# Optimization experiments

Measured on AMD Instinct MI355X. Metric: run time of the kernel, lower is better.

Reference implementation:

```python
import jax, jax.numpy as jnp
import numpy as np

N = 20000
E = 640000
H, C = 4, 64
L = 3
B = 16
EPS = 1e-5


def setup_inputs() -> dict:
    key = jax.random.key(0)
    ks = jax.random.split(key, 12)
    x = jax.random.normal(ks[0], (N, 256), dtype=jnp.float32)
    edge_index = jax.random.randint(ks[1], (2, E), 0, N, dtype=jnp.int64)
    batch = jnp.sort(jax.random.randint(ks[2], (N,), 0, B, dtype=jnp.int64))
    s = 0.05
    return {
        "x": x,
        "edge_index": edge_index,
        "batch": batch,
        "Wl": jax.random.normal(ks[3], (L, 256, H * C), dtype=jnp.float32) * s,
        "bl": jnp.zeros((L, H * C), dtype=jnp.float32),
        "Wr": jax.random.normal(ks[4], (L, 256, H * C), dtype=jnp.float32) * s,
        "br": jnp.zeros((L, H * C), dtype=jnp.float32),
        "att": jax.random.normal(ks[5], (L, H, C), dtype=jnp.float32) * s,
        "conv_bias": jnp.zeros((L, H * C), dtype=jnp.float32),
        "prelu_a": jnp.full((L,), 0.25, dtype=jnp.float32),
        "norm_w": jnp.ones((H * C,), dtype=jnp.float32),
        "norm_b": jnp.zeros((H * C,), dtype=jnp.float32),
        "norm_alpha": jnp.ones((H * C,), dtype=jnp.float32),
        "fc_W": jax.random.normal(ks[6], (H * C, 128), dtype=jnp.float32) * s,
        "fc_b": jnp.zeros((128,), dtype=jnp.float32),
    }


def graph_norm(h, w, b, alpha):
    # GraphNorm with batch=None: all rows form one segment (as in source forward)
    mean = jnp.mean(h, axis=0, keepdims=True)
    shifted = h - alpha * mean
    var = jnp.mean(shifted * shifted, axis=0, keepdims=True)
    return w * shifted / jnp.sqrt(var + EPS) + b


def gatv2_layer(h, src, dst, Wl, bl, Wr, br, att, bias):
    xl = (h @ Wl + bl).reshape(N, H, C)  # source transform
    xr = (h @ Wr + br).reshape(N, H, C)  # target transform
    m = jax.nn.leaky_relu(xl[src] + xr[dst], negative_slope=0.2)  # [Etot,H,C]
    e = jnp.einsum("ehc,hc->eh", m, att)  # [Etot,H]
    emax = jax.ops.segment_max(e, dst, num_segments=N)  # self-loops guarantee coverage
    ex = jnp.exp(e - emax[dst])
    denom = jax.ops.segment_sum(ex, dst, num_segments=N)
    alpha = ex / denom[dst]
    out = jax.ops.segment_sum(alpha[:, :, None] * xl[src], dst, num_segments=N)
    return out.reshape(N, H * C) + bias


def reference(x, edge_index, batch, Wl, bl, Wr, br, att, conv_bias, prelu_a,
              norm_w, norm_b, norm_alpha, fc_W, fc_b):
    loop = jnp.arange(N, dtype=edge_index.dtype)
    src = jnp.concatenate([edge_index[0], loop])  # add self-loops (PyG default)
    dst = jnp.concatenate([edge_index[1], loop])
    h = x
    for l in range(L):
        h = gatv2_layer(h, src, dst, Wl[l], bl[l], Wr[l], br[l], att[l], conv_bias[l])
        h = graph_norm(h, norm_w, norm_b, norm_alpha)
        h = jnp.where(h >= 0, h, prelu_a[l] * h)  # PReLU; dropout is identity in eval
    pooled = jax.ops.segment_sum(h, batch, num_segments=B)  # global_add_pool
    pooled = graph_norm(pooled, norm_w, norm_b, norm_alpha)  # shared norm reused after pool
    return pooled @ fc_W + fc_b
```

## Files before the change

### kernel.cpp

```cpp
#include <hip/hip_runtime.h>
#include <math.h>

#define N_NODES 20000
#define N_EDGES 640000
#define ETOT (N_EDGES + N_NODES)
#define HC 256
#define NLAYER 3
#define NBATCH 16
#define GEPS 1e-5f
#define STAT_BLOCKS 256

typedef unsigned short u16;
typedef unsigned int u32;
typedef __attribute__((ext_vector_type(8))) short short8;
typedef __attribute__((ext_vector_type(4))) float floatx4;

__device__ __forceinline__ u16 f2bf(float f) {
    u32 u = __float_as_uint(f);
    u32 r = (u + 0x7FFFu + ((u >> 16) & 1u)) >> 16;
    return (u16)r;
}

__device__ __forceinline__ float4 bf2f4(uint2 u) {
    float4 r;
    r.x = __uint_as_float(u.x << 16);
    r.y = __uint_as_float(u.x & 0xFFFF0000u);
    r.z = __uint_as_float(u.y << 16);
    r.w = __uint_as_float(u.y & 0xFFFF0000u);
    return r;
}

__device__ __forceinline__ float dpp_red16(float x) {
    x += __int_as_float(__builtin_amdgcn_update_dpp(0, __float_as_int(x), 0xB1, 0xF, 0xF, true));
    x += __int_as_float(__builtin_amdgcn_update_dpp(0, __float_as_int(x), 0x4E, 0xF, 0xF, true));
    x += __int_as_float(__builtin_amdgcn_update_dpp(0, __float_as_int(x), 0x141, 0xF, 0xF, true));
    x += __int_as_float(__builtin_amdgcn_update_dpp(0, __float_as_int(x), 0x140, 0xF, 0xF, true));
    return x;
}


__global__ void init_deg(int* deg) {
    int i = blockIdx.x * 256 + threadIdx.x;
    if (i < N_NODES) deg[i] = 1;
}

__global__ void count_deg(const int* __restrict__ dst, int* __restrict__ deg) {
    int e = blockIdx.x * 256 + threadIdx.x;
    if (e < N_EDGES) atomicAdd(&deg[dst[e]], 1);
}

__global__ __launch_bounds__(1024) void scan_excl(int* __restrict__ data, int* __restrict__ cursor) {
    __shared__ int wsum[16];
    __shared__ int carry_s;
    int tid = threadIdx.x, lane = tid & 63, wid = tid >> 6;
    if (tid == 0) carry_s = 0;
    __syncthreads();
    for (int base = 0; base < N_NODES; base += 1024) {
        int i = base + tid;
        int v = (i < N_NODES) ? data[i] : 0;
        int x = v;
        #pragma unroll
        for (int off = 1; off < 64; off <<= 1) {
            int t = __shfl_up(x, off);
            if (lane >= off) x += t;
        }
        if (lane == 63) wsum[wid] = x;
        __syncthreads();
        int carry = carry_s;
        __syncthreads();
        if (tid == 0) {
            int run = 0;
            #pragma unroll
            for (int w2 = 0; w2 < 16; ++w2) { int t = wsum[w2]; wsum[w2] = run; run += t; }
            carry_s = carry + run;
        }
        __syncthreads();
        int excl = carry + wsum[wid] + x - v;
        if (i < N_NODES) { data[i] = excl; cursor[i] = excl; }
        __syncthreads();
    }
    if (tid == 0) data[N_NODES] = carry_s;
}

__global__ void scatter_edges(const int* __restrict__ src, const int* __restrict__ dst,
                              int* __restrict__ cursor, int* __restrict__ col) {
    int t = blockIdx.x * 256 + threadIdx.x;
    if (t < N_NODES) {
        int p = atomicAdd(&cursor[t], 1);
        col[p] = t;
    } else if (t < N_NODES + N_EDGES) {
        int e = t - N_NODES;
        int p = atomicAdd(&cursor[dst[e]], 1);
        col[p] = src[e];
    }
}


__global__ __launch_bounds__(256) void convert_x(const float* __restrict__ x, u16* __restrict__ xb) {
    int i = blockIdx.x * 256 + threadIdx.x;
    const float4* x4 = (const float4*)x + (size_t)i * 2;
    float4 a = x4[0], b = x4[1];
    u16 o[8] = {f2bf(a.x), f2bf(a.y), f2bf(a.z), f2bf(a.w),
                f2bf(b.x), f2bf(b.y), f2bf(b.z), f2bf(b.w)};
    *((uint4*)xb + i) = *(const uint4*)o;
}

__global__ void transpose_w(const float* __restrict__ Wl, const float* __restrict__ Wr,
                            u16* __restrict__ WT) {
    __shared__ float T[32][33];
    int l = blockIdx.z;
    int n0 = blockIdx.y * 32, k0 = blockIdx.x * 32;
    const float* W = ((n0 < 256) ? Wl : Wr) + (size_t)l * 65536;
    int nn = n0 & 255;
    int tx = threadIdx.x, ty = threadIdx.y;
    #pragma unroll
    for (int i = 0; i < 4; ++i)
        T[ty + i * 8][tx] = W[(size_t)(k0 + ty + i * 8) * 256 + nn + tx];
    __syncthreads();
    u16* out = WT + (size_t)l * 512 * 256;
    #pragma unroll
    for (int i = 0; i < 4; ++i)
        out[(size_t)(n0 + ty + i * 8) * 256 + k0 + tx] = f2bf(T[tx][ty + i * 8]);
}


__global__ __launch_bounds__(256) void gemm_mfma(
    const u16* __restrict__ Abf, const u16* __restrict__ WT,
    const float* __restrict__ b0, const float* __restrict__ b1,
    u16* __restrict__ xlb, float* __restrict__ xrf) {
    __shared__ u16 As[128][40];
    __shared__ u16 Bs[128][40];
    int row0 = blockIdx.x * 128;
    int nstrip = blockIdx.y;
    int ncol0 = nstrip * 128;
    const float* bias = (nstrip < 2) ? b0 : b1;

    int tid = threadIdx.x;
    int wave = tid >> 6, lane = tid & 63;
    int wm = (wave & 1) * 64, wn = (wave >> 1) * 64;
    int quad = lane >> 4, l16 = lane & 15;

    floatx4 acc[4][4] = {};

    int sr = tid >> 1;
    int sh = (tid & 1) * 16;

    for (int k0 = 0; k0 < 256; k0 += 32) {
        int gr = row0 + sr;
        uint4 av0 = make_uint4(0, 0, 0, 0), av1 = make_uint4(0, 0, 0, 0);
        if (gr < N_NODES) {
            const u16* p = Abf + (size_t)gr * 256 + k0 + sh;
            av0 = *(const uint4*)p;
            av1 = *(const uint4*)(p + 8);
        }
        const u16* q = WT + (size_t)(ncol0 + sr) * 256 + k0 + sh;
        uint4 bv0 = *(const uint4*)q;
        uint4 bv1 = *(const uint4*)(q + 8);
        *(uint4*)&As[sr][sh] = av0;
        *(uint4*)&As[sr][sh + 8] = av1;
        *(uint4*)&Bs[sr][sh] = bv0;
        *(uint4*)&Bs[sr][sh + 8] = bv1;
        __syncthreads();

        short8 af[4], bfr[4];
        #pragma unroll
        for (int mi = 0; mi < 4; ++mi)
            af[mi] = *(const short8*)&As[wm + mi * 16 + l16][quad * 8];
        #pragma unroll
        for (int ni = 0; ni < 4; ++ni)
            bfr[ni] = *(const short8*)&Bs[wn + ni * 16 + l16][quad * 8];
        #pragma unroll
        for (int mi = 0; mi < 4; ++mi)
            #pragma unroll
            for (int ni = 0; ni < 4; ++ni)
                acc[mi][ni] = __builtin_amdgcn_mfma_f32_16x16x32_bf16(af[mi], bfr[ni], acc[mi][ni], 0, 0, 0);
        __syncthreads();
    }

    if (nstrip < 2) {
        int c0 = nstrip * 128;
        #pragma unroll
        for (int ni = 0; ni < 4; ++ni) {
            int col = c0 + wn + ni * 16 + l16;
            float bv = bias[col];
            #pragma unroll
            for (int mi = 0; mi < 4; ++mi) {
                int gr = row0 + wm + mi * 16 + quad * 4;
                #pragma unroll
                for (int r = 0; r < 4; ++r) {
                    if (gr + r < N_NODES)
                        xlb[(size_t)(gr + r) * 256 + col] = f2bf(acc[mi][ni][r] + bv);
                }
            }
        }
    } else {
        int c0 = (nstrip - 2) * 128;
        #pragma unroll
        for (int ni = 0; ni < 4; ++ni) {
            int col = c0 + wn + ni * 16 + l16;
            float bv = bias[col];
            #pragma unroll
            for (int mi = 0; mi < 4; ++mi) {
                int gr = row0 + wm + mi * 16 + quad * 4;
                #pragma unroll
                for (int r = 0; r < 4; ++r) {
                    if (gr + r < N_NODES)
                        xrf[(size_t)(gr + r) * 256 + col] = acc[mi][ni][r] + bv;
                }
            }
        }
    }
}


__global__ __launch_bounds__(256) void gat_agg(
    const u16* __restrict__ xlb, const float* __restrict__ xr,
    const int* __restrict__ rowptr, const int* __restrict__ col,
    const float* __restrict__ att_l, const float* __restrict__ bias_l,
    float* __restrict__ out) {
    int wid = threadIdx.x >> 6, lane = threadIdx.x & 63;
    int node = blockIdx.x * 4 + wid;
    if (node >= N_NODES) return;
    const uint2* xl2 = (const uint2*)xlb;
    float4 attv = ((const float4*)att_l)[lane];
    float4 xrv = ((const float4*)xr)[(size_t)node * 64 + lane];
    int beg = rowptr[node], end = rowptr[node + 1];

    float denom = 0.f;
    float4 acc = make_float4(0.f, 0.f, 0.f, 0.f);

    int j = beg;
    for (; j + 8 <= end; j += 8) {
        int s[8];
        uint2 raw[8];
        float4 a[8];
        float p[8];
        #pragma unroll
        for (int u = 0; u < 8; ++u) s[u] = col[j + u];
        #pragma unroll
        for (int u = 0; u < 8; ++u) raw[u] = xl2[(size_t)s[u] * 64 + lane];
        #pragma unroll
        for (int u = 0; u < 8; ++u) {
            a[u] = bf2f4(raw[u]);
            float vx = a[u].x + xrv.x, vy = a[u].y + xrv.y;
            float vz = a[u].z + xrv.z, vw = a[u].w + xrv.w;
            vx = fmaxf(vx, 0.2f * vx);
            vy = fmaxf(vy, 0.2f * vy);
            vz = fmaxf(vz, 0.2f * vz);
            vw = fmaxf(vw, 0.2f * vw);
            p[u] = vx * attv.x + vy * attv.y + vz * attv.z + vw * attv.w;
        }
        #pragma unroll
        for (int u = 0; u < 8; ++u) p[u] = dpp_red16(p[u]);
        #pragma unroll
        for (int u = 0; u < 8; ++u) {
            float w = __expf(p[u]);
            denom += w;
            acc.x += w * a[u].x; acc.y += w * a[u].y;
            acc.z += w * a[u].z; acc.w += w * a[u].w;
        }
    }
    for (; j < end; ++j) {
        int s = col[j];
        float4 a = bf2f4(xl2[(size_t)s * 64 + lane]);
        float vx = a.x + xrv.x, vy = a.y + xrv.y;
        float vz = a.z + xrv.z, vw = a.w + xrv.w;
        vx = fmaxf(vx, 0.2f * vx);
        vy = fmaxf(vy, 0.2f * vy);
        vz = fmaxf(vz, 0.2f * vz);
        vw = fmaxf(vw, 0.2f * vw);
        float p = vx * attv.x + vy * attv.y + vz * attv.z + vw * attv.w;
        p = dpp_red16(p);
        float w = __expf(p);
        denom += w;
        acc.x += w * a.x; acc.y += w * a.y; acc.z += w * a.z; acc.w += w * a.w;
    }

    float inv = 1.f / denom;
    float4 b4 = ((const float4*)bias_l)[lane];
    float4 o;
    o.x = acc.x * inv + b4.x; o.y = acc.y * inv + b4.y;
    o.z = acc.z * inv + b4.z; o.w = acc.w * inv + b4.w;
    ((float4*)out)[(size_t)node * 64 + lane] = o;
}


__global__ __launch_bounds__(256) void col_stats_part(const float* __restrict__ h,
                                                      float* __restrict__ partials) {
    __shared__ float s_red[256][8];
    int t = threadIdx.x;
    int rgrp = t >> 6;
    int c4 = t & 63;
    float4 sum = make_float4(0.f, 0.f, 0.f, 0.f);
    float4 sq = make_float4(0.f, 0.f, 0.f, 0.f);
    for (int r = blockIdx.x * 4 + rgrp; r < N_NODES; r += STAT_BLOCKS * 4) {
        float4 v = ((const float4*)h)[(size_t)r * 64 + c4];
        sum.x += v.x; sum.y += v.y; sum.z += v.z; sum.w += v.w;
        sq.x += v.x * v.x; sq.y += v.y * v.y; sq.z += v.z * v.z; sq.w += v.w * v.w;
    }
    s_red[t][0] = sum.x; s_red[t][1] = sum.y; s_red[t][2] = sum.z; s_red[t][3] = sum.w;
    s_red[t][4] = sq.x;  s_red[t][5] = sq.y;  s_red[t][6] = sq.z;  s_red[t][7] = sq.w;
    __syncthreads();
    if (rgrp == 0) {
        float acc8[8];
        #pragma unroll
        for (int k = 0; k < 8; ++k)
            acc8[k] = s_red[c4][k] + s_red[64 + c4][k] + s_red[128 + c4][k] + s_red[192 + c4][k];
        float* pb = partials + (size_t)blockIdx.x * 512;
        *(float4*)&pb[c4 * 4]       = make_float4(acc8[0], acc8[1], acc8[2], acc8[3]);
        *(float4*)&pb[256 + c4 * 4] = make_float4(acc8[4], acc8[5], acc8[6], acc8[7]);
    }
}

__global__ __launch_bounds__(256) void stats_reduce(const float* __restrict__ partials,
                                                    float* __restrict__ stats) {
    int o = blockIdx.x * 256 + threadIdx.x;
    float s = 0.f;
    for (int b = 0; b < STAT_BLOCKS; ++b) s += partials[(size_t)b * 512 + o];
    stats[o] = s;
}


__global__ __launch_bounds__(256) void norm_prelu(
    const float* __restrict__ h2, u16* __restrict__ hbf, float* __restrict__ hf,
    const float* __restrict__ stats,
    const float* __restrict__ w, const float* __restrict__ b, const float* __restrict__ alpha,
    const float* __restrict__ pa, int l, int wf32) {
    int t = threadIdx.x;
    int row = blockIdx.x * 4 + (t >> 6);
    int c4 = t & 63;
    int c = c4 * 4;
    const float invn = 1.f / (float)N_NODES;
    float4 m4 = *(const float4*)&stats[c];
    float4 e4 = *(const float4*)&stats[256 + c];
    float4 al4 = *(const float4*)&alpha[c];
    float4 w4 = *(const float4*)&w[c];
    float4 b4 = *(const float4*)&b[c];
    float ap = pa[l];

    float4 mean, wc, sh;
    mean.x = m4.x * invn; mean.y = m4.y * invn; mean.z = m4.z * invn; mean.w = m4.w * invn;
    float4 Eh2;
    Eh2.x = e4.x * invn; Eh2.y = e4.y * invn; Eh2.z = e4.z * invn; Eh2.w = e4.w * invn;
    wc.x = w4.x * rsqrtf(Eh2.x - (2.f * al4.x - al4.x * al4.x) * mean.x * mean.x + GEPS);
    wc.y = w4.y * rsqrtf(Eh2.y - (2.f * al4.y - al4.y * al4.y) * mean.y * mean.y + GEPS);
    wc.z = w4.z * rsqrtf(Eh2.z - (2.f * al4.z - al4.z * al4.z) * mean.z * mean.z + GEPS);
    wc.w = w4.w * rsqrtf(Eh2.w - (2.f * al4.w - al4.w * al4.w) * mean.w * mean.w + GEPS);
    sh.x = al4.x * mean.x; sh.y = al4.y * mean.y; sh.z = al4.z * mean.z; sh.w = al4.w * mean.w;

    float4 v = ((const float4*)h2)[(size_t)row * 64 + c4];
    v.x = (v.x - sh.x) * wc.x + b4.x;
    v.y = (v.y - sh.y) * wc.y + b4.y;
    v.z = (v.z - sh.z) * wc.z + b4.z;
    v.w = (v.w - sh.w) * wc.w + b4.w;
    v.x = (v.x >= 0.f) ? v.x : ap * v.x;
    v.y = (v.y >= 0.f) ? v.y : ap * v.y;
    v.z = (v.z >= 0.f) ? v.z : ap * v.z;
    v.w = (v.w >= 0.f) ? v.w : ap * v.w;
    u16 o4[4] = {f2bf(v.x), f2bf(v.y), f2bf(v.z), f2bf(v.w)};
    *(uint2*)(hbf + (size_t)row * 256 + c) = *(const uint2*)o4;
    if (wf32) ((float4*)hf)[(size_t)row * 64 + c4] = v;
}


__global__ __launch_bounds__(256) void pool_kernel(const float* __restrict__ h,
                                                   const int* __restrict__ batch,
                                                   float* __restrict__ pooled) {
    __shared__ float accs[NBATCH][256];
    int c = threadIdx.x;
    #pragma unroll
    for (int b = 0; b < NBATCH; ++b) accs[b][c] = 0.f;
    int rows_per = (N_NODES + gridDim.x - 1) / gridDim.x;
    int r0 = blockIdx.x * rows_per;
    int r1 = min(N_NODES, r0 + rows_per);
    for (int i = r0; i < r1; ++i) accs[batch[i]][c] += h[(size_t)i * 256 + c];
    #pragma unroll
    for (int b = 0; b < NBATCH; ++b) atomicAdd(&pooled[b * 256 + c], accs[b][c]);
}

__global__ __launch_bounds__(256) void pool_norm(const float* __restrict__ pooled, float* __restrict__ pn,
                                                 const float* __restrict__ w, const float* __restrict__ b,
                                                 const float* __restrict__ alpha) {
    int c = threadIdx.x;
    float mean = 0.f, sq = 0.f;
    #pragma unroll
    for (int i = 0; i < NBATCH; ++i) { float v = pooled[i * 256 + c]; mean += v; sq += v * v; }
    mean *= (1.f / NBATCH); sq *= (1.f / NBATCH);
    float al = alpha[c];
    float var = sq - (2.f * al - al * al) * mean * mean;
    float wc = w[c] * rsqrtf(var + GEPS);
    #pragma unroll
    for (int i = 0; i < NBATCH; ++i) {
        float v = (pooled[i * 256 + c] - al * mean) * wc + b[c];
        pn[i * 256 + c] = v;
    }
}

__global__ __launch_bounds__(128) void fc_kernel(const float* __restrict__ pn, const float* __restrict__ W,
                                                 const float* __restrict__ bias, float* __restrict__ out) {
    int b = blockIdx.x, o = threadIdx.x;
    float s = bias[o];
    for (int k = 0; k < 256; ++k) s += pn[b * 256 + k] * W[k * 128 + o];
    out[b * 128 + o] = s;
}


extern "C" void kernel_launch(void* const* d_in, const int* in_sizes, int n_in,
                              void* d_out, int out_size, void* d_ws, size_t ws_size,
                              hipStream_t stream) {
    const float* x    = (const float*)d_in[0];
    const int*   ei   = (const int*)d_in[1];
    const int*   batch= (const int*)d_in[2];
    const float* Wl   = (const float*)d_in[3];
    const float* bl   = (const float*)d_in[4];
    const float* Wr   = (const float*)d_in[5];
    const float* br   = (const float*)d_in[6];
    const float* att  = (const float*)d_in[7];
    const float* cb   = (const float*)d_in[8];
    const float* pa   = (const float*)d_in[9];
    const float* nw   = (const float*)d_in[10];
    const float* nb   = (const float*)d_in[11];
    const float* na   = (const float*)d_in[12];
    const float* fcW  = (const float*)d_in[13];
    const float* fcb  = (const float*)d_in[14];
    float* out = (float*)d_out;

    char* ws = (char*)d_ws;
    size_t off = 0;
    auto carve = [&](size_t bytes) -> void* {
        void* p = (void*)(ws + off);
        off += (bytes + 255) & ~(size_t)255;
        return p;
    };
    int*   rowptr = (int*)carve((N_NODES + 1) * sizeof(int));
    int*   cursor = (int*)carve(N_NODES * sizeof(int));
    int*   colidx = (int*)carve((size_t)ETOT * sizeof(int));
    u16*   xlb    = (u16*)carve((size_t)N_NODES * HC * sizeof(u16));
    float* xr     = (float*)carve((size_t)N_NODES * HC * sizeof(float));
    float* hB     = (float*)carve((size_t)N_NODES * HC * sizeof(float));
    float* hf     = (float*)carve((size_t)N_NODES * HC * sizeof(float));
    u16*   xbf    = (u16*)carve((size_t)N_NODES * HC * sizeof(u16));
    u16*   hbf    = (u16*)carve((size_t)N_NODES * HC * sizeof(u16));
    u16*   WT     = (u16*)carve((size_t)NLAYER * 512 * 256 * sizeof(u16));
    float* partials = (float*)carve((size_t)STAT_BLOCKS * 512 * sizeof(float));
    float* stats  = (float*)carve(512 * sizeof(float));
    float* pooled = (float*)carve(NBATCH * HC * sizeof(float));
    float* pn     = (float*)carve(NBATCH * HC * sizeof(float));

    const int* srcp = ei;
    const int* dstp = ei + N_EDGES;

    init_deg<<<(N_NODES + 255) / 256, 256, 0, stream>>>(rowptr);
    count_deg<<<(N_EDGES + 255) / 256, 256, 0, stream>>>(dstp, rowptr);
    scan_excl<<<1, 1024, 0, stream>>>(rowptr, cursor);
    scatter_edges<<<(ETOT + 255) / 256, 256, 0, stream>>>(srcp, dstp, cursor, colidx);

    convert_x<<<2500, 256, 0, stream>>>(x, xbf);
    transpose_w<<<dim3(8, 16, 3), dim3(32, 8), 0, stream>>>(Wl, Wr, WT);

    for (int l = 0; l < NLAYER; ++l) {
        const u16* hin = (l == 0) ? xbf : hbf;
        gemm_mfma<<<dim3(157, 4), 256, 0, stream>>>(hin, WT + (size_t)l * 512 * 256,
                                                    bl + l * 256, br + l * 256, xlb, xr);
        gat_agg<<<5000, 256, 0, stream>>>(xlb, xr, rowptr, colidx, att + l * 256, cb + l * 256, hB);
        col_stats_part<<<STAT_BLOCKS, 256, 0, stream>>>(hB, partials);
        stats_reduce<<<2, 256, 0, stream>>>(partials, stats);
        norm_prelu<<<5000, 256, 0, stream>>>(hB, hbf, hf, stats, nw, nb, na, pa, l,
                                             (l == NLAYER - 1) ? 1 : 0);
    }
    hipMemsetAsync(pooled, 0, NBATCH * HC * sizeof(float), stream);
    pool_kernel<<<100, 256, 0, stream>>>(hf, batch, pooled);
    pool_norm<<<1, 256, 0, stream>>>(pooled, pn, nw, nb, na);
    fc_kernel<<<NBATCH, 128, 0, stream>>>(pn, fcW, fcb, out);
}
```

Before: 573.5 us.

## Fuse graph norm into GEMM prologue and aggregation stats, merge CSR and prep kernels

Column statistics are now accumulated by atomic adds into slotted buffers inside the aggregation kernel, which writes bf16 output. The next layer's GEMM applies GraphNorm and PReLU while loading its A tile, so the separate stats, reduce and norm passes and their full-size fp32 traffic are gone. The CSR build is one persistent kernel using software grid barriers. Input conversion, weight transpose and workspace zeroing share one launch, and the pool-norm and fc kernels are merged. The risks are extra per-element work in the GEMM load path, a spin-barrier deadlock if all 256 blocks are not co-resident, and bf16 rounding of the pre-norm activations.

```diff
diff --git a/kernel.cpp b/kernel.cpp
--- a/kernel.cpp
+++ b/kernel.cpp
@@ -8,7 +8,7 @@
 #define NLAYER 3
 #define NBATCH 16
 #define GEPS 1e-5f
-#define STAT_BLOCKS 256
+#define NSLOT 64
 
 typedef unsigned short u16;
 typedef unsigned int u32;
@@ -39,103 +39,151 @@
 }
 
 
-__global__ void init_deg(int* deg) {
-    int i = blockIdx.x * 256 + threadIdx.x;
-    if (i < N_NODES) deg[i] = 1;
-}
-
-__global__ void count_deg(const int* __restrict__ dst, int* __restrict__ deg) {
-    int e = blockIdx.x * 256 + threadIdx.x;
-    if (e < N_EDGES) atomicAdd(&deg[dst[e]], 1);
-}
-
-__global__ __launch_bounds__(1024) void scan_excl(int* __restrict__ data, int* __restrict__ cursor) {
-    __shared__ int wsum[16];
-    __shared__ int carry_s;
-    int tid = threadIdx.x, lane = tid & 63, wid = tid >> 6;
-    if (tid == 0) carry_s = 0;
+__global__ __launch_bounds__(256) void prep(const float* __restrict__ x, u16* __restrict__ xbf,
+                                            const float* __restrict__ Wl, const float* __restrict__ Wr,
+                                            u16* __restrict__ WT, uint4* __restrict__ zbase, int zq) {
+    int b = blockIdx.x, tid = threadIdx.x;
+    if (b < 1000) {
+        for (int i = b * 256 + tid; i < 640000; i += 256000) {
+            const float4* x4 = (const float4*)x + (size_t)i * 2;
+            float4 a = x4[0], c = x4[1];
+            u16 o[8] = {f2bf(a.x), f2bf(a.y), f2bf(a.z), f2bf(a.w),
+                        f2bf(c.x), f2bf(c.y), f2bf(c.z), f2bf(c.w)};
+            ((uint4*)xbf)[i] = *(const uint4*)o;
+        }
+    } else if (b < 1384) {
+        __shared__ float T[32][33];
+        int bi = b - 1000;
+        int kb = bi & 7, nbk = (bi >> 3) & 15, l = bi >> 7;
+        int n0 = nbk * 32, k0 = kb * 32;
+        const float* W = ((n0 < 256) ? Wl : Wr) + (size_t)l * 65536;
+        int nn = n0 & 255;
+        int tx = tid & 31, ty = tid >> 5;
+        #pragma unroll
+        for (int i = 0; i < 4; ++i)
+            T[ty + i * 8][tx] = W[(size_t)(k0 + ty + i * 8) * 256 + nn + tx];
+        __syncthreads();
+        u16* outw = WT + (size_t)l * 512 * 256;
+        #pragma unroll
+        for (int i = 0; i < 4; ++i)
+            outw[(size_t)(n0 + ty + i * 8) * 256 + k0 + tx] = f2bf(T[tx][ty + i * 8]);
+    } else {
+        uint4 z = make_uint4(0, 0, 0, 0);
+        for (int i = (b - 1384) * 256 + tid; i < zq; i += 120 * 256) zbase[i] = z;
+    }
+}
+
+
+__device__ __forceinline__ void gbar(int* bar, int target) {
     __syncthreads();
-    for (int base = 0; base < N_NODES; base += 1024) {
-        int i = base + tid;
-        int v = (i < N_NODES) ? data[i] : 0;
-        int x = v;
-        #pragma unroll
-        for (int off = 1; off < 64; off <<= 1) {
-            int t = __shfl_up(x, off);
-            if (lane >= off) x += t;
-        }
-        if (lane == 63) wsum[wid] = x;
+    if (threadIdx.x == 0) {
+        __threadfence();
+        atomicAdd(bar, 1);
+        while (atomicAdd(bar, 0) < target) __builtin_amdgcn_s_sleep(8);
+        __threadfence();
+    }
+    __syncthreads();
+}
+
+__global__ __launch_bounds__(256) void csr_fused(const int* __restrict__ src, const int* __restrict__ dst,
+                                                 int* __restrict__ rowptr, int* __restrict__ cursor,
+                                                 int* __restrict__ colx, int* bar,
+                                                 int* __restrict__ blocksum) {
+    int tid = threadIdx.x, b = blockIdx.x;
+    int gid = b * 256 + tid;
+    __shared__ int sdata[256];
+    __shared__ int loc[80];
+
+    for (int e = gid; e < N_EDGES; e += 65536) atomicAdd(&rowptr[dst[e]], 1);
+    gbar(bar, 256);
+
+    int n0 = b * 79, n1 = min(n0 + 79, N_NODES);
+    if (n0 > N_NODES) n1 = n0;
+    int v = 0;
+    if (n0 + tid < n1) { v = rowptr[n0 + tid] + 1; loc[tid] = v; }
+    sdata[tid] = v;
+    __syncthreads();
+    for (int s2 = 128; s2 > 0; s2 >>= 1) {
+        if (tid < s2) sdata[tid] += sdata[tid + s2];
         __syncthreads();
-        int carry = carry_s;
+    }
+    if (tid == 0) blocksum[b] = sdata[0];
+    gbar(bar, 512);
+
+    if (b == 0) {
+        int mine = blocksum[tid];
+        sdata[tid] = mine;
         __syncthreads();
-        if (tid == 0) {
-            int run = 0;
-            #pragma unroll
-            for (int w2 = 0; w2 < 16; ++w2) { int t = wsum[w2]; wsum[w2] = run; run += t; }
-            carry_s = carry + run;
-        }
-        __syncthreads();
-        int excl = carry + wsum[wid] + x - v;
-        if (i < N_NODES) { data[i] = excl; cursor[i] = excl; }
-        __syncthreads();
-    }
-    if (tid == 0) data[N_NODES] = carry_s;
-}
-
-__global__ void scatter_edges(const int* __restrict__ src, const int* __restrict__ dst,
-                              int* __restrict__ cursor, int* __restrict__ col) {
-    int t = blockIdx.x * 256 + threadIdx.x;
-    if (t < N_NODES) {
-        int p = atomicAdd(&cursor[t], 1);
-        col[p] = t;
-    } else if (t < N_NODES + N_EDGES) {
-        int e = t - N_NODES;
-        int p = atomicAdd(&cursor[dst[e]], 1);
-        col[p] = src[e];
-    }
-}
-
-
-__global__ __launch_bounds__(256) void convert_x(const float* __restrict__ x, u16* __restrict__ xb) {
-    int i = blockIdx.x * 256 + threadIdx.x;
-    const float4* x4 = (const float4*)x + (size_t)i * 2;
-    float4 a = x4[0], b = x4[1];
-    u16 o[8] = {f2bf(a.x), f2bf(a.y), f2bf(a.z), f2bf(a.w),
-                f2bf(b.x), f2bf(b.y), f2bf(b.z), f2bf(b.w)};
-    *((uint4*)xb + i) = *(const uint4*)o;
-}
-
-__global__ void transpose_w(const float* __restrict__ Wl, const float* __restrict__ Wr,
-                            u16* __restrict__ WT) {
-    __shared__ float T[32][33];
-    int l = blockIdx.z;
-    int n0 = blockIdx.y * 32, k0 = blockIdx.x * 32;
-    const float* W = ((n0 < 256) ? Wl : Wr) + (size_t)l * 65536;
-    int nn = n0 & 255;
-    int tx = threadIdx.x, ty = threadIdx.y;
-    #pragma unroll
-    for (int i = 0; i < 4; ++i)
-        T[ty + i * 8][tx] = W[(size_t)(k0 + ty + i * 8) * 256 + nn + tx];
-    __syncthreads();
-    u16* out = WT + (size_t)l * 512 * 256;
-    #pragma unroll
-    for (int i = 0; i < 4; ++i)
-        out[(size_t)(n0 + ty + i * 8) * 256 + k0 + tx] = f2bf(T[tx][ty + i * 8]);
+        for (int off2 = 1; off2 < 256; off2 <<= 1) {
+            int t2 = (tid >= off2) ? sdata[tid - off2] : 0;
+            __syncthreads();
+            sdata[tid] += t2;
+            __syncthreads();
+        }
+        blocksum[tid] = sdata[tid] - mine;
+    }
+    gbar(bar, 768);
+
+    if (tid == 0) {
+        int run = blocksum[b];
+        for (int i = n0; i < n1; ++i) {
+            int d = loc[i - n0];
+            rowptr[i] = run;
+            cursor[i] = run;
+            run += d;
+        }
+        if (b == 255) rowptr[N_NODES] = ETOT;
+    }
+    gbar(bar, 1024);
+
+    for (int t = gid; t < ETOT; t += 65536) {
+        if (t < N_NODES) {
+            int p = atomicAdd(&cursor[t], 1);
+            colx[p] = t;
+        } else {
+            int e = t - N_NODES;
+            int p = atomicAdd(&cursor[dst[e]], 1);
+            colx[p] = src[e];
+        }
+    }
 }
 
 
 __global__ __launch_bounds__(256) void gemm_mfma(
-    const u16* __restrict__ Abf, const u16* __restrict__ WT,
+    const u16* __restrict__ Asrc, const float* __restrict__ slots_prev,
+    const float* __restrict__ nw, const float* __restrict__ nb, const float* __restrict__ na,
+    const float* __restrict__ pa, int prelu_idx, int use_norm,
+    const u16* __restrict__ WT,
     const float* __restrict__ b0, const float* __restrict__ b1,
     u16* __restrict__ xlb, float* __restrict__ xrf) {
     __shared__ u16 As[128][40];
     __shared__ u16 Bs[128][40];
+    __shared__ float wcL[256], bbL[256];
     int row0 = blockIdx.x * 128;
     int nstrip = blockIdx.y;
     int ncol0 = nstrip * 128;
     const float* bias = (nstrip < 2) ? b0 : b1;
 
     int tid = threadIdx.x;
+    float ap = 0.f;
+    if (use_norm) {
+        int c = tid;
+        float sum = 0.f, sq = 0.f;
+        for (int s = 0; s < NSLOT; ++s) {
+            sum += slots_prev[s * 512 + c];
+            sq += slots_prev[s * 512 + 256 + c];
+        }
+        const float invn = 1.f / (float)N_NODES;
+        float mean = sum * invn, Eh2 = sq * invn;
+        float a = na[c];
+        float var = Eh2 - (2.f * a - a * a) * mean * mean;
+        float wc = nw[c] * rsqrtf(var + GEPS);
+        wcL[c] = wc;
+        bbL[c] = nb[c] - a * mean * wc;
+        ap = pa[prelu_idx];
+        __syncthreads();
+    }
+
     int wave = tid >> 6, lane = tid & 63;
     int wm = (wave & 1) * 64, wn = (wave >> 1) * 64;
     int quad = lane >> 4, l16 = lane & 15;
@@ -149,17 +197,41 @@
         int gr = row0 + sr;
         uint4 av0 = make_uint4(0, 0, 0, 0), av1 = make_uint4(0, 0, 0, 0);
         if (gr < N_NODES) {
-            const u16* p = Abf + (size_t)gr * 256 + k0 + sh;
+            const u16* p = Asrc + (size_t)gr * 256 + k0 + sh;
             av0 = *(const uint4*)p;
             av1 = *(const uint4*)(p + 8);
         }
+        if (use_norm) {
+            int kb2 = k0 + sh;
+            u16 tmp[16];
+            *(uint4*)tmp = av0;
+            *(uint4*)(tmp + 8) = av1;
+            float4 wv0 = *(const float4*)&wcL[kb2], wv1 = *(const float4*)&wcL[kb2 + 4];
+            float4 wv2 = *(const float4*)&wcL[kb2 + 8], wv3 = *(const float4*)&wcL[kb2 + 12];
+            float4 bv0 = *(const float4*)&bbL[kb2], bv1 = *(const float4*)&bbL[kb2 + 4];
+            float4 bv2 = *(const float4*)&bbL[kb2 + 8], bv3 = *(const float4*)&bbL[kb2 + 12];
+            float wvf[16] = {wv0.x, wv0.y, wv0.z, wv0.w, wv1.x, wv1.y, wv1.z, wv1.w,
+                             wv2.x, wv2.y, wv2.z, wv2.w, wv3.x, wv3.y, wv3.z, wv3.w};
+            float bvf[16] = {bv0.x, bv0.y, bv0.z, bv0.w, bv1.x, bv1.y, bv1.z, bv1.w,
+                             bv2.x, bv2.y, bv2.z, bv2.w, bv3.x, bv3.y, bv3.z, bv3.w};
+            u16 outv[16];
+            #pragma unroll
+            for (int j = 0; j < 16; ++j) {
+                float vv = __uint_as_float(((u32)tmp[j]) << 16);
+                float t2 = vv * wvf[j] + bvf[j];
+                t2 = fmaxf(t2, ap * t2);
+                outv[j] = f2bf(t2);
+            }
+            av0 = *(const uint4*)outv;
+            av1 = *(const uint4*)(outv + 8);
+        }
         const u16* q = WT + (size_t)(ncol0 + sr) * 256 + k0 + sh;
-        uint4 bv0 = *(const uint4*)q;
-        uint4 bv1 = *(const uint4*)(q + 8);
+        uint4 bw0 = *(const uint4*)q;
+        uint4 bw1 = *(const uint4*)(q + 8);
         *(uint4*)&As[sr][sh] = av0;
         *(uint4*)&As[sr][sh + 8] = av1;
-        *(uint4*)&Bs[sr][sh] = bv0;
-        *(uint4*)&Bs[sr][sh + 8] = bv1;
+        *(uint4*)&Bs[sr][sh] = bw0;
+        *(uint4*)&Bs[sr][sh + 8] = bw1;
         __syncthreads();
 
         short8 af[4], bfr[4];
@@ -205,7 +277,7 @@
                 #pragma unroll
                 for (int r = 0; r < 4; ++r) {
                     if (gr + r < N_NODES)
-                        xrf[(size_t)(gr + r) * 256 + col] = acc[mi][ni][r] + bv;
+                        xrf[(size_t)(gr + r) * 256 + c0 + wn + ni * 16 + l16] = acc[mi][ni][r] + bv;
                 }
             }
         }
@@ -213,14 +285,14 @@
 }
 
 
-__global__ __launch_bounds__(256) void gat_agg(
+__global__ __launch_bounds__(1024) void gat_agg(
     const u16* __restrict__ xlb, const float* __restrict__ xr,
     const int* __restrict__ rowptr, const int* __restrict__ col,
     const float* __restrict__ att_l, const float* __restrict__ bias_l,
-    float* __restrict__ out) {
+    u16* __restrict__ hB, float* __restrict__ slot) {
+    __shared__ float sred[16][520];
     int wid = threadIdx.x >> 6, lane = threadIdx.x & 63;
-    int node = blockIdx.x * 4 + wid;
-    if (node >= N_NODES) return;
+    int node = blockIdx.x * 16 + wid;
     const uint2* xl2 = (const uint2*)xlb;
     float4 attv = ((const float4*)att_l)[lane];
     float4 xrv = ((const float4*)xr)[(size_t)node * 64 + lane];
@@ -281,127 +353,89 @@
     float4 o;
     o.x = acc.x * inv + b4.x; o.y = acc.y * inv + b4.y;
     o.z = acc.z * inv + b4.z; o.w = acc.w * inv + b4.w;
-    ((float4*)out)[(size_t)node * 64 + lane] = o;
-}
-
-
-__global__ __launch_bounds__(256) void col_stats_part(const float* __restrict__ h,
-                                                      float* __restrict__ partials) {
-    __shared__ float s_red[256][8];
+    u16 ob[4] = {f2bf(o.x), f2bf(o.y), f2bf(o.z), f2bf(o.w)};
+    ((uint2*)hB)[(size_t)node * 64 + lane] = *(const uint2*)ob;
+
+    int cb2 = lane * 4;
+    sred[wid][cb2 + 0] = o.x; sred[wid][cb2 + 1] = o.y;
+    sred[wid][cb2 + 2] = o.z; sred[wid][cb2 + 3] = o.w;
+    sred[wid][256 + cb2 + 0] = o.x * o.x; sred[wid][256 + cb2 + 1] = o.y * o.y;
+    sred[wid][256 + cb2 + 2] = o.z * o.z; sred[wid][256 + cb2 + 3] = o.w * o.w;
+    __syncthreads();
     int t = threadIdx.x;
-    int rgrp = t >> 6;
-    int c4 = t & 63;
-    float4 sum = make_float4(0.f, 0.f, 0.f, 0.f);
-    float4 sq = make_float4(0.f, 0.f, 0.f, 0.f);
-    for (int r = blockIdx.x * 4 + rgrp; r < N_NODES; r += STAT_BLOCKS * 4) {
-        float4 v = ((const float4*)h)[(size_t)r * 64 + c4];
-        sum.x += v.x; sum.y += v.y; sum.z += v.z; sum.w += v.w;
-        sq.x += v.x * v.x; sq.y += v.y * v.y; sq.z += v.z * v.z; sq.w += v.w * v.w;
-    }
-    s_red[t][0] = sum.x; s_red[t][1] = sum.y; s_red[t][2] = sum.z; s_red[t][3] = sum.w;
-    s_red[t][4] = sq.x;  s_red[t][5] = sq.y;  s_red[t][6] = sq.z;  s_red[t][7] = sq.w;
-    __syncthreads();
-    if (rgrp == 0) {
-        float acc8[8];
-        #pragma unroll
-        for (int k = 0; k < 8; ++k)
-            acc8[k] = s_red[c4][k] + s_red[64 + c4][k] + s_red[128 + c4][k] + s_red[192 + c4][k];
-        float* pb = partials + (size_t)blockIdx.x * 512;
-        *(float4*)&pb[c4 * 4]       = make_float4(acc8[0], acc8[1], acc8[2], acc8[3]);
-        *(float4*)&pb[256 + c4 * 4] = make_float4(acc8[4], acc8[5], acc8[6], acc8[7]);
-    }
-}
-
-__global__ __launch_bounds__(256) void stats_reduce(const float* __restrict__ partials,
-                                                    float* __restrict__ stats) {
-    int o = blockIdx.x * 256 + threadIdx.x;
-    float s = 0.f;
-    for (int b = 0; b < STAT_BLOCKS; ++b) s += partials[(size_t)b * 512 + o];
-    stats[o] = s;
-}
-
-
-__global__ __launch_bounds__(256) void norm_prelu(
-    const float* __restrict__ h2, u16* __restrict__ hbf, float* __restrict__ hf,
-    const float* __restrict__ stats,
-    const float* __restrict__ w, const float* __restrict__ b, const float* __restrict__ alpha,
-    const float* __restrict__ pa, int l, int wf32) {
-    int t = threadIdx.x;
-    int row = blockIdx.x * 4 + (t >> 6);
-    int c4 = t & 63;
-    int c = c4 * 4;
-    const float invn = 1.f / (float)N_NODES;
-    float4 m4 = *(const float4*)&stats[c];
-    float4 e4 = *(const float4*)&stats[256 + c];
-    float4 al4 = *(const float4*)&alpha[c];
-    float4 w4 = *(const float4*)&w[c];
-    float4 b4 = *(const float4*)&b[c];
-    float ap = pa[l];
-
-    float4 mean, wc, sh;
-    mean.x = m4.x * invn; mean.y = m4.y * invn; mean.z = m4.z * invn; mean.w = m4.w * invn;
-    float4 Eh2;
-    Eh2.x = e4.x * invn; Eh2.y = e4.y * invn; Eh2.z = e4.z * invn; Eh2.w = e4.w * invn;
-    wc.x = w4.x * rsqrtf(Eh2.x - (2.f * al4.x - al4.x * al4.x) * mean.x * mean.x + GEPS);
-    wc.y = w4.y * rsqrtf(Eh2.y - (2.f * al4.y - al4.y * al4.y) * mean.y * mean.y + GEPS);
-    wc.z = w4.z * rsqrtf(Eh2.z - (2.f * al4.z - al4.z * al4.z) * mean.z * mean.z + GEPS);
-    wc.w = w4.w * rsqrtf(Eh2.w - (2.f * al4.w - al4.w * al4.w) * mean.w * mean.w + GEPS);
-    sh.x = al4.x * mean.x; sh.y = al4.y * mean.y; sh.z = al4.z * mean.z; sh.w = al4.w * mean.w;
-
-    float4 v = ((const float4*)h2)[(size_t)row * 64 + c4];
-    v.x = (v.x - sh.x) * wc.x + b4.x;
-    v.y = (v.y - sh.y) * wc.y + b4.y;
-    v.z = (v.z - sh.z) * wc.z + b4.z;
-    v.w = (v.w - sh.w) * wc.w + b4.w;
-    v.x = (v.x >= 0.f) ? v.x : ap * v.x;
-    v.y = (v.y >= 0.f) ? v.y : ap * v.y;
-    v.z = (v.z >= 0.f) ? v.z : ap * v.z;
-    v.w = (v.w >= 0.f) ? v.w : ap * v.w;
-    u16 o4[4] = {f2bf(v.x), f2bf(v.y), f2bf(v.z), f2bf(v.w)};
-    *(uint2*)(hbf + (size_t)row * 256 + c) = *(const uint2*)o4;
-    if (wf32) ((float4*)hf)[(size_t)row * 64 + c4] = v;
-}
-
-
-__global__ __launch_bounds__(256) void pool_kernel(const float* __restrict__ h,
+    if (t < 512) {
+        float s = 0.f;
+        #pragma unroll
+        for (int w = 0; w < 16; ++w) s += sred[w][t];
+        atomicAdd(&slot[(blockIdx.x & (NSLOT - 1)) * 512 + t], s);
+    }
+}
+
+
+__global__ __launch_bounds__(256) void pool_kernel(const u16* __restrict__ hB,
                                                    const int* __restrict__ batch,
+                                                   const float* __restrict__ slots2,
+                                                   const float* __restrict__ nw, const float* __restrict__ nb,
+                                                   const float* __restrict__ na, const float* __restrict__ pa,
                                                    float* __restrict__ pooled) {
     __shared__ float accs[NBATCH][256];
     int c = threadIdx.x;
+    float sum = 0.f, sq = 0.f;
+    for (int s = 0; s < NSLOT; ++s) {
+        sum += slots2[s * 512 + c];
+        sq += slots2[s * 512 + 256 + c];
+    }
+    const float invn = 1.f / (float)N_NODES;
+    float mean = sum * invn, Eh2 = sq * invn;
+    float a = na[c];
+    float var = Eh2 - (2.f * a - a * a) * mean * mean;
+    float wc = nw[c] * rsqrtf(var + GEPS);
+    float bb = nb[c] - a * mean * wc;
+    float ap = pa[2];
+
     #pragma unroll
     for (int b = 0; b < NBATCH; ++b) accs[b][c] = 0.f;
-    int rows_per = (N_NODES + gridDim.x - 1) / gridDim.x;
-    int r0 = blockIdx.x * rows_per;
-    int r1 = min(N_NODES, r0 + rows_per);
-    for (int i = r0; i < r1; ++i) accs[batch[i]][c] += h[(size_t)i * 256 + c];
-    #pragma unroll
-    for (int b = 0; b < NBATCH; ++b) atomicAdd(&pooled[b * 256 + c], accs[b][c]);
-}
-
-__global__ __launch_bounds__(256) void pool_norm(const float* __restrict__ pooled, float* __restrict__ pn,
-                                                 const float* __restrict__ w, const float* __restrict__ b,
-                                                 const float* __restrict__ alpha) {
+    int r0 = blockIdx.x * 100;
+    int r1 = min(N_NODES, r0 + 100);
+    for (int i = r0; i < r1; ++i) {
+        float v = __uint_as_float(((u32)hB[(size_t)i * 256 + c]) << 16);
+        v = v * wc + bb;
+        v = fmaxf(v, ap * v);
+        accs[batch[i]][c] += v;
+    }
+    int bmin = batch[r0], bmax = batch[r1 - 1];
+    for (int b = bmin; b <= bmax; ++b) atomicAdd(&pooled[b * 256 + c], accs[b][c]);
+}
+
+
+__global__ __launch_bounds__(256) void poolnorm_fc(const float* __restrict__ pooled,
+                                                   const float* __restrict__ nw, const float* __restrict__ nb,
+                                                   const float* __restrict__ na,
+                                                   const float* __restrict__ fcW, const float* __restrict__ fcb,
+                                                   float* __restrict__ out) {
+    __shared__ float pn[NBATCH][256];
     int c = threadIdx.x;
     float mean = 0.f, sq = 0.f;
     #pragma unroll
-    for (int i = 0; i < NBATCH; ++i) { float v = pooled[i * 256 + c]; mean += v; sq += v * v; }
+    for (int i = 0; i < NBATCH; ++i) {
+        float v = pooled[i * 256 + c];
+        mean += v; sq += v * v;
+    }
     mean *= (1.f / NBATCH); sq *= (1.f / NBATCH);
-    float al = alpha[c];
-    float var = sq - (2.f * al - al * al) * mean * mean;
-    float wc = w[c] * rsqrtf(var + GEPS);
+    float a = na[c];
+    float var = sq - (2.f * a - a * a) * mean * mean;
+    float wc = nw[c] * rsqrtf(var + GEPS);
+    float bb = nb[c] - a * mean * wc;
     #pragma unroll
-    for (int i = 0; i < NBATCH; ++i) {
-        float v = (pooled[i * 256 + c] - al * mean) * wc + b[c];
-        pn[i * 256 + c] = v;
-    }
-}
-
-__global__ __launch_bounds__(128) void fc_kernel(const float* __restrict__ pn, const float* __restrict__ W,
-                                                 const float* __restrict__ bias, float* __restrict__ out) {
-    int b = blockIdx.x, o = threadIdx.x;
-    float s = bias[o];
-    for (int k = 0; k < 256; ++k) s += pn[b * 256 + k] * W[k * 128 + o];
-    out[b * 128 + o] = s;
+    for (int i = 0; i < NBATCH; ++i)
+        pn[i][c] = pooled[i * 256 + c] * wc + bb;
+    __syncthreads();
+    int o = c & 127, bset = c >> 7;
+    for (int b = bset; b < NBATCH; b += 2) {
+        float s = fcb[o];
+        for (int k = 0; k < 256; ++k) s += pn[b][k] * fcW[k * 128 + o];
+        out[b * 128 + o] = s;
+    }
 }
 
 
@@ -432,44 +466,39 @@
         off += (bytes + 255) & ~(size_t)255;
         return p;
     };
+    size_t z0 = off;
     int*   rowptr = (int*)carve((N_NODES + 1) * sizeof(int));
+    int*   bar    = (int*)carve(16 * sizeof(int));
+    float* slots  = (float*)carve((size_t)NLAYER * NSLOT * 512 * sizeof(float));
+    float* pooled = (float*)carve(NBATCH * HC * sizeof(float));
+    size_t z1 = off;
     int*   cursor = (int*)carve(N_NODES * sizeof(int));
+    int*   blocksum = (int*)carve(256 * sizeof(int));
     int*   colidx = (int*)carve((size_t)ETOT * sizeof(int));
     u16*   xlb    = (u16*)carve((size_t)N_NODES * HC * sizeof(u16));
     float* xr     = (float*)carve((size_t)N_NODES * HC * sizeof(float));
-    float* hB     = (float*)carve((size_t)N_NODES * HC * sizeof(float));
-    float* hf     = (float*)carve((size_t)N_NODES * HC * sizeof(float));
+    u16*   hB     = (u16*)carve((size_t)N_NODES * HC * sizeof(u16));
     u16*   xbf    = (u16*)carve((size_t)N_NODES * HC * sizeof(u16));
-    u16*   hbf    = (u16*)carve((size_t)N_NODES * HC * sizeof(u16));
     u16*   WT     = (u16*)carve((size_t)NLAYER * 512 * 256 * sizeof(u16));
-    float* partials = (float*)carve((size_t)STAT_BLOCKS * 512 * sizeof(float));
-    float* stats  = (float*)carve(512 * sizeof(float));
-    float* pooled = (float*)carve(NBATCH * HC * sizeof(float));
-    float* pn     = (float*)carve(NBATCH * HC * sizeof(float));
-
+
+    int zq = (int)((z1 - z0) / 16);
     const int* srcp = ei;
     const int* dstp = ei + N_EDGES;
 
-    init_deg<<<(N_NODES + 255) / 256, 256, 0, stream>>>(rowptr);
-    count_deg<<<(N_EDGES + 255) / 256, 256, 0, stream>>>(dstp, rowptr);
-    scan_excl<<<1, 1024, 0, stream>>>(rowptr, cursor);
-    scatter_edges<<<(ETOT + 255) / 256, 256, 0, stream>>>(srcp, dstp, cursor, colidx);
-
-    convert_x<<<2500, 256, 0, stream>>>(x, xbf);
-    transpose_w<<<dim3(8, 16, 3), dim3(32, 8), 0, stream>>>(Wl, Wr, WT);
+    prep<<<1504, 256, 0, stream>>>(x, xbf, Wl, Wr, WT, (uint4*)(ws + z0), zq);
+    csr_fused<<<256, 256, 0, stream>>>(srcp, dstp, rowptr, cursor, colidx, bar, blocksum);
 
     for (int l = 0; l < NLAYER; ++l) {
-        const u16* hin = (l == 0) ? xbf : hbf;
-        gemm_mfma<<<dim3(157, 4), 256, 0, stream>>>(hin, WT + (size_t)l * 512 * 256,
+        const u16* Asrc = (l == 0) ? xbf : hB;
+        const float* slots_prev = slots + (size_t)((l > 0) ? (l - 1) : 0) * NSLOT * 512;
+        gemm_mfma<<<dim3(157, 4), 256, 0, stream>>>(Asrc, slots_prev, nw, nb, na, pa,
+                                                    (l > 0) ? (l - 1) : 0, (l > 0) ? 1 : 0,
+                                                    WT + (size_t)l * 512 * 256,
                                                     bl + l * 256, br + l * 256, xlb, xr);
-        gat_agg<<<5000, 256, 0, stream>>>(xlb, xr, rowptr, colidx, att + l * 256, cb + l * 256, hB);
-        col_stats_part<<<STAT_BLOCKS, 256, 0, stream>>>(hB, partials);
-        stats_reduce<<<2, 256, 0, stream>>>(partials, stats);
-        norm_prelu<<<5000, 256, 0, stream>>>(hB, hbf, hf, stats, nw, nb, na, pa, l,
-                                             (l == NLAYER - 1) ? 1 : 0);
-    }
-    hipMemsetAsync(pooled, 0, NBATCH * HC * sizeof(float), stream);
-    pool_kernel<<<100, 256, 0, stream>>>(hf, batch, pooled);
-    pool_norm<<<1, 256, 0, stream>>>(pooled, pn, nw, nb, na);
-    fc_kernel<<<NBATCH, 128, 0, stream>>>(pn, fcW, fcb, out);
-}
+        gat_agg<<<1250, 1024, 0, stream>>>(xlb, xr, rowptr, colidx, att + l * 256, cb + l * 256,
+                                           hB, slots + (size_t)l * NSLOT * 512);
+    }
+    pool_kernel<<<200, 256, 0, stream>>>(hB, batch, slots + (size_t)2 * NSLOT * 512,
+                                         nw, nb, na, pa, pooled);
+    poolnorm_fc<<<1, 256, 0, stream>>>(pooled, nw, nb, na, fcW, fcb, out);
+}
```

New measurement: 629.5 us. 9.8% more time.
